# Performance work log

Measured on AMD Instinct MI355X. Metric: run time of the kernel, lower is better.

The kernel has to match this reference:

```python
import jax, jax.numpy as jnp
import numpy as np

N, E = 20000, 320000
IN, HID, R, HEADS = 128, 256, 4, 4
C = HID // HEADS  # per-head dim


def setup_inputs() -> dict:
    key = jax.random.key(0)
    ks = jax.random.split(key, 20)
    g = lambda k, s, sc=0.05: jax.random.normal(k, s, jnp.float32) * sc
    return {
        'x': g(ks[0], (N, IN), 1.0),
        'edge_index': jax.random.randint(ks[1], (2, E), 0, N),
        'edge_type': jax.random.randint(ks[2], (E,), 0, R),
        'h_prev': g(ks[3], (N, HID), 1.0),
        # RGCN layer 1: relation weights, root weight, bias
        'W1': g(ks[4], (R, IN, HID)), 'root1': g(ks[5], (IN, HID)), 'b1': jnp.zeros((HID,), jnp.float32),
        # RGCN layer 2
        'W2': g(ks[6], (R, HID, HID)), 'root2': g(ks[7], (HID, HID)), 'b2': jnp.zeros((HID,), jnp.float32),
        # TransformerConv linears (query/key/value/skip), each Linear(HID, HEADS*C)
        'Wq': g(ks[8], (HID, HID)), 'bq': jnp.zeros((HID,), jnp.float32),
        'Wk': g(ks[9], (HID, HID)), 'bk': jnp.zeros((HID,), jnp.float32),
        'Wv': g(ks[10], (HID, HID)), 'bv': jnp.zeros((HID,), jnp.float32),
        'Wskip': g(ks[11], (HID, HID)), 'bskip': jnp.zeros((HID,), jnp.float32),
        # GRUCell (torch layout: [3*HID, in], gates ordered r, z, n)
        'W_ih': g(ks[12], (3 * HID, HID)), 'b_ih': jnp.zeros((3 * HID,), jnp.float32),
        'W_hh': g(ks[13], (3 * HID, HID)), 'b_hh': jnp.zeros((3 * HID,), jnp.float32),
    }


def rgcn(x, src, dst, etype, W, Wroot, b):
    # PyG RGCNConv: out_i = x_i @ Wroot + b + sum_r mean_{j in N_r(i)} x_j @ W_r
    n = x.shape[0]
    out = x @ Wroot + b
    xs = x[src]  # [E, F_in]
    for r in range(W.shape[0]):  # small fixed relation count
        mask = (etype == r).astype(x.dtype)  # [E]
        msg = (xs @ W[r]) * mask[:, None]  # [E, F_out]
        agg = jax.ops.segment_sum(msg, dst, num_segments=n)
        cnt = jax.ops.segment_sum(mask, dst, num_segments=n)
        out = out + agg / jnp.maximum(cnt, 1.0)[:, None]
    return out


def transformer_conv(x, src, dst, Wq, bq, Wk, bk, Wv, bv, Wskip, bskip):
    # PyG TransformerConv, concat=True, root_weight=True
    n = x.shape[0]
    q = (x @ Wq + bq).reshape(n, HEADS, C)
    k = (x @ Wk + bk).reshape(n, HEADS, C)
    v = (x @ Wv + bv).reshape(n, HEADS, C)
    score = jnp.einsum('ehc,ehc->eh', q[dst], k[src]) * (1.0 / np.sqrt(C))  # [E, H]
    smax = jax.ops.segment_max(score, dst, num_segments=n)  # [N, H]
    ex = jnp.exp(score - smax[dst])
    denom = jax.ops.segment_sum(ex, dst, num_segments=n)
    alpha = ex / jnp.maximum(denom[dst], 1e-16)  # edge softmax per dst node
    out = jax.ops.segment_sum(alpha[:, :, None] * v[src], dst, num_segments=n)  # [N, H, C]
    return out.reshape(n, HEADS * C) + x @ Wskip + bskip


def gru_cell(xi, h, W_ih, b_ih, W_hh, b_hh):
    gi = xi @ W_ih.T + b_ih
    gh = h @ W_hh.T + b_hh
    ir, iz, inn = jnp.split(gi, 3, axis=1)
    hr, hz, hn = jnp.split(gh, 3, axis=1)
    r = jax.nn.sigmoid(ir + hr)
    z = jax.nn.sigmoid(iz + hz)
    nw = jnp.tanh(inn + r * hn)
    return (1.0 - z) * nw + z * h


def reference(x, edge_index, edge_type, h_prev, W1, root1, b1, W2, root2, b2,
              Wq, bq, Wk, bk, Wv, bv, Wskip, bskip, W_ih, b_ih, W_hh, b_hh):
    src, dst = edge_index[0], edge_index[1]
    h = jax.nn.relu(rgcn(x, src, dst, edge_type, W1, root1, b1))
    h = jax.nn.relu(rgcn(h, src, dst, edge_type, W2, root2, b2))
    h = transformer_conv(h, src, dst, Wq, bq, Wk, bk, Wv, bv, Wskip, bskip)
    h = gru_cell(h, h_prev, W_ih, b_ih, W_hh, b_hh)
    return h
```

## Files before the change

### kernel.cpp

```cpp
#include <hip/hip_runtime.h>
#include <hip/hip_bf16.h>
#include <stdint.h>

#define N_NODES 20000
#define E_EDGES 320000
#define IN_F    128
#define HIDF    256
#define R_REL   4
#define NRKEYS  (N_NODES*R_REL)
#define SCAN_BLOCKS 80

typedef __attribute__((ext_vector_type(8))) short  short8;
typedef __attribute__((ext_vector_type(4))) float  floatx4;

__device__ __forceinline__ float bf2f(__hip_bfloat16 v){ return __bfloat162float(v); }
__device__ __forceinline__ __hip_bfloat16 f2bf(float v){ return __float2bfloat16(v); }
__device__ __forceinline__ float bfbits2f(unsigned short u){ return __uint_as_float(((unsigned)u)<<16); }
__device__ __forceinline__ unsigned short f2bfbits(float v){
    __hip_bfloat16 h = __float2bfloat16(v);
    return *(unsigned short*)&h;
}
__device__ __forceinline__ unsigned pack_bf2(float a, float b){
    return (unsigned)f2bfbits(a) | ((unsigned)f2bfbits(b) << 16);
}

__device__ __forceinline__ void gload_lds16(const void* g, void* l)
{
    __builtin_amdgcn_global_load_lds((const __attribute__((address_space(1))) void*)g,
                                     (__attribute__((address_space(3))) void*)l, 16, 0, 0);
}

template<int N>
__device__ __forceinline__ void wait_vm()
{
    if constexpr (N == 0)      asm volatile("s_waitcnt vmcnt(0)" ::: "memory");
    else if constexpr (N == 3) asm volatile("s_waitcnt vmcnt(3)" ::: "memory");
    else if constexpr (N == 4) asm volatile("s_waitcnt vmcnt(4)" ::: "memory");
    else if constexpr (N == 5) asm volatile("s_waitcnt vmcnt(5)" ::: "memory");
    else                       asm volatile("s_waitcnt vmcnt(0)" ::: "memory");
}

__device__ __forceinline__ int2 xcd_swizzle()
{
    int gx = gridDim.x, gy = gridDim.y;
    int nwg = gx * gy;
    int lin = blockIdx.x + gx * blockIdx.y;
    int q = nwg >> 3, r = nwg & 7;
    int k = lin & 7, i = lin >> 3;
    int j = (k < r ? k*(q+1) : r*(q+1) + (k-r)*q) + i;
    return make_int2(j / gy, j % gy);
}

__global__ void count_kernel(const int* __restrict__ ei, const int* __restrict__ et,
                             int* __restrict__ cnt)
{
    int e = blockIdx.x*256 + threadIdx.x;
    if (e >= E_EDGES) return;
    int dst = ei[E_EDGES + e];
    atomicAdd(&cnt[dst*R_REL + et[e]], 1);
}

__global__ __launch_bounds__(1024) void scan_reduce_kernel(const int* __restrict__ cnt,
                                                           int* __restrict__ blocksum)
{
    int ix = blockIdx.x*1024 + threadIdx.x;
    int v = (ix < NRKEYS) ? cnt[ix] : 0;
    #pragma unroll
    for (int o=32;o>0;o>>=1) v += __shfl_xor(v, o, 64);
    __shared__ int wsum[16];
    int wave = threadIdx.x >> 6, lane = threadIdx.x & 63;
    if (lane == 0) wsum[wave] = v;
    __syncthreads();
    if (threadIdx.x == 0) {
        int s = 0;
        #pragma unroll
        for (int w=0;w<16;w++) s += wsum[w];
        blocksum[blockIdx.x] = s;
    }
}

__global__ __launch_bounds__(128) void scan_sums_kernel(const int* __restrict__ blocksum,
                                                        int* __restrict__ blockoff)
{
    __shared__ int s[128];
    int t = threadIdx.x;
    int v = (t < SCAN_BLOCKS) ? blocksum[t] : 0;
    s[t] = v; __syncthreads();
    for (int off=1; off<128; off<<=1) {
        int u = (t>=off) ? s[t-off] : 0;
        __syncthreads();
        s[t] += u;
        __syncthreads();
    }
    if (t < SCAN_BLOCKS) blockoff[t] = s[t] - v;
}

__global__ __launch_bounds__(1024) void scan_apply_kernel(const int* __restrict__ cnt,
                                                          const int* __restrict__ blockoff,
                                                          int* __restrict__ row_ptr,
                                                          int* __restrict__ cursor)
{
    __shared__ int s[1024];
    int t = threadIdx.x;
    int ix = blockIdx.x*1024 + t;
    int v = (ix < NRKEYS) ? cnt[ix] : 0;
    s[t] = v; __syncthreads();
    for (int off=1; off<1024; off<<=1) {
        int u = (t>=off) ? s[t-off] : 0;
        __syncthreads();
        s[t] += u;
        __syncthreads();
    }
    if (ix < NRKEYS) {
        int excl = blockoff[blockIdx.x] + s[t] - v;
        row_ptr[ix] = excl;
        cursor[ix]  = excl;
        if (ix == NRKEYS-1) row_ptr[NRKEYS] = excl + v;
    }
}

__global__ void fill_kernel(const int* __restrict__ ei, const int* __restrict__ et,
                            int* __restrict__ cursor, int* __restrict__ csr_src)
{
    int e = blockIdx.x*256 + threadIdx.x;
    if (e >= E_EDGES) return;
    int src = ei[e];
    int dst = ei[E_EDGES + e];
    int key = dst*R_REL + et[e];
    int pos = atomicAdd(&cursor[key], 1);
    csr_src[pos] = src;
}

__global__ void make_b1t(const float* __restrict__ root1,
                         const float* __restrict__ W1,
                         __hip_bfloat16* __restrict__ B1t)
{
    int idx = blockIdx.x*256 + threadIdx.x;
    if (idx >= 256*640) return;
    int n = idx / 640, k = idx % 640;
    float v;
    if (k < 128) v = root1[k*256 + n];
    else         v = W1[(k-128)*256 + n];
    B1t[idx] = f2bf(v);
}

__global__ void make_b2t(const float* __restrict__ root2,
                         const float* __restrict__ W2,
                         __hip_bfloat16* __restrict__ B2t)
{
    int idx = blockIdx.x*256 + threadIdx.x;
    if (idx >= 256*1280) return;
    int n = idx / 1280, k = idx % 1280;
    float v;
    if (k < 256) v = root2[k*256 + n];
    else         v = W2[(k-256)*256 + n];
    B2t[idx] = f2bf(v);
}

__global__ void make_b3t(const float* __restrict__ Wq, const float* __restrict__ Wk,
                         const float* __restrict__ Wv, const float* __restrict__ Wsk,
                         const float* __restrict__ bq, const float* __restrict__ bk,
                         const float* __restrict__ bv, const float* __restrict__ bsk,
                         __hip_bfloat16* __restrict__ B3t, float* __restrict__ bias3)
{
    int idx = blockIdx.x*256 + threadIdx.x;
    if (idx >= 1024*256) return;
    int n = idx / 256, k = idx % 256;
    int g = n >> 8, nn = n & 255;
    const float* W = (g==0)?Wq:(g==1)?Wk:(g==2)?Wv:Wsk;
    B3t[idx] = f2bf(W[k*256 + nn]);
    if (k == 0) {
        const float* B = (g==0)?bq:(g==1)?bk:(g==2)?bv:bsk;
        bias3[n] = B[nn];
    }
}

__global__ void cvt_f32_bf16(const float* __restrict__ in, __hip_bfloat16* __restrict__ out, int n)
{
    int i = blockIdx.x*256 + threadIdx.x;
    if (i < n) out[i] = f2bf(in[i]);
}

__global__ __launch_bounds__(256) void agg1_kernel(const float* __restrict__ x,
                                                   const int* __restrict__ row_ptr,
                                                   const int* __restrict__ csr_src,
                                                   __hip_bfloat16* __restrict__ A1)
{
    int b = blockIdx.x*4 + (threadIdx.x >> 6);
    int lane = threadIdx.x & 63;
    int i = b >> 2, r = b & 3;
    int e0 = row_ptr[b], e1 = row_ptr[b+1];
    float sx0=0.f,sy0=0.f, sx1=0.f,sy1=0.f, sx2=0.f,sy2=0.f, sx3=0.f,sy3=0.f;
    int e = e0;
    for (; e+4 <= e1; e += 4) {
        int i0=csr_src[e], i1=csr_src[e+1], i2=csr_src[e+2], i3=csr_src[e+3];
        float2 v0 = *(const float2*)(x + (size_t)i0*IN_F + lane*2);
        float2 v1 = *(const float2*)(x + (size_t)i1*IN_F + lane*2);
        float2 v2 = *(const float2*)(x + (size_t)i2*IN_F + lane*2);
        float2 v3 = *(const float2*)(x + (size_t)i3*IN_F + lane*2);
        sx0+=v0.x; sy0+=v0.y; sx1+=v1.x; sy1+=v1.y;
        sx2+=v2.x; sy2+=v2.y; sx3+=v3.x; sy3+=v3.y;
    }
    for (; e < e1; e++) {
        int i0 = csr_src[e];
        float2 v = *(const float2*)(x + (size_t)i0*IN_F + lane*2);
        sx0+=v.x; sy0+=v.y;
    }
    float sx = (sx0+sx1)+(sx2+sx3);
    float sy = (sy0+sy1)+(sy2+sy3);
    float inv = (e1>e0) ? 1.f/(float)(e1-e0) : 0.f;
    *(unsigned*)(A1 + (size_t)i*640 + 128 + r*128 + lane*2) = pack_bf2(sx*inv, sy*inv);
    if (r == 0) {
        float2 v = *(const float2*)(x + (size_t)i*IN_F + lane*2);
        *(unsigned*)(A1 + (size_t)i*640 + lane*2) = pack_bf2(v.x, v.y);
    }
}

__global__ __launch_bounds__(256) void agg2_kernel(const int* __restrict__ row_ptr,
                                                   const int* __restrict__ csr_src,
                                                   __hip_bfloat16* __restrict__ A2)
{
    int b = blockIdx.x*4 + (threadIdx.x >> 6);
    int lane = threadIdx.x & 63;
    int i = b >> 2, r = b & 3;
    int e0 = row_ptr[b], e1 = row_ptr[b+1];
    float a0=0.f,a1=0.f,a2=0.f,a3=0.f;
    float b0=0.f,b1=0.f,b2=0.f,b3=0.f;
    float c0=0.f,c1=0.f,c2=0.f,c3=0.f;
    float d0=0.f,d1=0.f,d2=0.f,d3=0.f;
    int e = e0;
    for (; e+4 <= e1; e += 4) {
        int i0=csr_src[e], i1=csr_src[e+1], i2=csr_src[e+2], i3=csr_src[e+3];
        ushort4 u0 = *(const ushort4*)(A2 + (size_t)i0*1280 + lane*4);
        ushort4 u1 = *(const ushort4*)(A2 + (size_t)i1*1280 + lane*4);
        ushort4 u2 = *(const ushort4*)(A2 + (size_t)i2*1280 + lane*4);
        ushort4 u3 = *(const ushort4*)(A2 + (size_t)i3*1280 + lane*4);
        a0+=bfbits2f(u0.x); a1+=bfbits2f(u0.y); a2+=bfbits2f(u0.z); a3+=bfbits2f(u0.w);
        b0+=bfbits2f(u1.x); b1+=bfbits2f(u1.y); b2+=bfbits2f(u1.z); b3+=bfbits2f(u1.w);
        c0+=bfbits2f(u2.x); c1+=bfbits2f(u2.y); c2+=bfbits2f(u2.z); c3+=bfbits2f(u2.w);
        d0+=bfbits2f(u3.x); d1+=bfbits2f(u3.y); d2+=bfbits2f(u3.z); d3+=bfbits2f(u3.w);
    }
    for (; e < e1; e++) {
        int i0 = csr_src[e];
        ushort4 u = *(const ushort4*)(A2 + (size_t)i0*1280 + lane*4);
        a0+=bfbits2f(u.x); a1+=bfbits2f(u.y); a2+=bfbits2f(u.z); a3+=bfbits2f(u.w);
    }
    float s0=(a0+b0)+(c0+d0), s1=(a1+b1)+(c1+d1), s2=(a2+b2)+(c2+d2), s3=(a3+b3)+(c3+d3);
    float inv = (e1>e0) ? 1.f/(float)(e1-e0) : 0.f;
    uint2 w;
    w.x = pack_bf2(s0*inv, s1*inv);
    w.y = pack_bf2(s2*inv, s3*inv);
    *(uint2*)(A2 + (size_t)i*1280 + 256 + r*256 + lane*4) = w;
}

template<int MI>
__device__ __forceinline__ void gemm_bt_body(const __hip_bfloat16* __restrict__ A, int lda,
                                             const __hip_bfloat16* __restrict__ Bt,
                                             const float* __restrict__ bias,
                                             __hip_bfloat16* __restrict__ C, int ldc,
                                             int M, int K, int relu,
                                             int tile_m, int tile_n,
                                             __hip_bfloat16* lds_a, __hip_bfloat16* lds_b)
{
    constexpr int A_ELEMS = MI*1024;
    constexpr int B_ELEMS = 4096;
    constexpr int L = MI/2 + 2;
    const int tid  = threadIdx.x;
    const int wave = tid >> 6;
    const int lane = tid & 63;
    const int wm = wave >> 1, wn = wave & 1;
    const int fm = lane & 15;
    const int q  = lane >> 4;
    const int sw = (q ^ ((fm >> 1) & 3)) * 8;

    floatx4 acc[MI][4];
    #pragma unroll
    for (int i=0;i<MI;i++)
        #pragma unroll
        for (int j=0;j<4;j++) acc[i][j] = (floatx4){0.f,0.f,0.f,0.f};

    const int srow   = lane >> 2;
    const int schunk = lane & 3;
    size_t a_goff[MI/2];
    #pragma unroll
    for (int s = 0; s < MI/2; ++s) {
        int r = (s*4 + wave)*16 + srow;
        int c = schunk ^ ((r >> 1) & 3);
        a_goff[s] = (size_t)min(tile_m + r, M-1)*lda + c*8;
    }
    size_t b_goff[2];
    #pragma unroll
    for (int s = 0; s < 2; ++s) {
        int r = (s*4 + wave)*16 + srow;
        int c = schunk ^ ((r >> 1) & 3);
        b_goff[s] = (size_t)(tile_n + r)*K + c*8;
    }

    const int nt = K >> 5;

    auto issue = [&](int t, int bufi) {
        const int kn = t << 5;
        #pragma unroll
        for (int s = 0; s < MI/2; ++s)
            gload_lds16(A + a_goff[s] + kn, lds_a + bufi*A_ELEMS + (s*4 + wave)*512);
        #pragma unroll
        for (int s = 0; s < 2; ++s)
            gload_lds16(Bt + b_goff[s] + kn, lds_b + bufi*B_ELEMS + (s*4 + wave)*512);
    };

    issue(0, 0);
    if (nt > 1) { issue(1, 1); wait_vm<L>(); }
    else        { wait_vm<0>(); }
    __builtin_amdgcn_s_barrier();

    int cur = 0, nx2 = 2;
    for (int t = 0; t < nt; ++t) {
        if (t + 2 < nt) issue(t + 2, nx2);

        const __hip_bfloat16* la = lds_a + cur*A_ELEMS;
        const __hip_bfloat16* lb = lds_b + cur*B_ELEMS;
        short8 afr[MI], bfr[4];
        #pragma unroll
        for (int i=0;i<MI;i++)
            afr[i] = *(const short8*)(la + (wm*(MI*16) + i*16 + fm)*32 + sw);
        #pragma unroll
        for (int j=0;j<4;j++)
            bfr[j] = *(const short8*)(lb + (wn*64 + j*16 + fm)*32 + sw);

        __builtin_amdgcn_s_setprio(1);
        #pragma unroll
        for (int i=0;i<MI;i++)
            #pragma unroll
            for (int j=0;j<4;j++)
                acc[i][j] = __builtin_amdgcn_mfma_f32_16x16x32_bf16(afr[i], bfr[j], acc[i][j], 0,0,0);
        __builtin_amdgcn_s_setprio(0);

        if (t + 1 < nt) {
            if (t + 2 < nt) wait_vm<L>();
            else            wait_vm<0>();
            __builtin_amdgcn_s_barrier();
            cur = (cur == 2) ? 0 : cur + 1;
            nx2 = (nx2 == 2) ? 0 : nx2 + 1;
        }
    }

    const int crow_base = tile_m + wm*(MI*16);
    const int ccol_base = tile_n + wn*64;
    #pragma unroll
    for (int i=0;i<MI;i++) {
        #pragma unroll
        for (int j=0;j<4;j++) {
            int c  = ccol_base + j*16 + fm;
            float bb = bias[c];
            #pragma unroll
            for (int rg=0; rg<4; rg++) {
                int r = crow_base + i*16 + q*4 + rg;
                if (r < M) {
                    float v = acc[i][j][rg] + bb;
                    if (relu) v = fmaxf(v, 0.f);
                    C[(size_t)r*ldc + c] = f2bf(v);
                }
            }
        }
    }
}

template<int MI>
__global__ __launch_bounds__(256) void gemm_bt_t(const __hip_bfloat16* __restrict__ A, int lda,
                                                 const __hip_bfloat16* __restrict__ Bt,
                                                 const float* __restrict__ bias,
                                                 __hip_bfloat16* __restrict__ C, int ldc,
                                                 int M, int K, int relu)
{
    __shared__ __align__(16) __hip_bfloat16 lds_a[3*MI*1024];
    __shared__ __align__(16) __hip_bfloat16 lds_b[3*4096];
    int2 xy = xcd_swizzle();
    gemm_bt_body<MI>(A, lda, Bt, bias, C, ldc, M, K, relu,
                     xy.x*(MI*32), xy.y*128, lds_a, lds_b);
}

__global__ __launch_bounds__(256) void gemm_gru_fused(
    const __hip_bfloat16* __restrict__ A0,
    const __hip_bfloat16* __restrict__ A1,
    const __hip_bfloat16* __restrict__ Bt0,
    const __hip_bfloat16* __restrict__ Bt1,
    const float* __restrict__ b_ih, const float* __restrict__ b_hh,
    const float* __restrict__ hprev, float* __restrict__ out)
{
    constexpr int BUF_ELEMS = 10240;
    __shared__ __align__(16) __hip_bfloat16 lds[3*BUF_ELEMS];
    int2 xy = xcd_swizzle();
    const int tile_m = xy.x * 64;
    const int c0     = xy.y * 32;
    const int tid = threadIdx.x, wave = tid >> 6, lane = tid & 63;
    const int fm = lane & 15, q = lane >> 4;
    const int sw = (q ^ ((fm >> 1) & 3)) * 8;

    const int sub = lane >> 2, ch = lane & 3;
    const __hip_bfloat16* gsrc[5];
    int dstoff[5];
    #pragma unroll
    for (int s = 0; s < 5; ++s) {
        int seg = wave*5 + s;
        if (seg < 8) {
            int fr = seg*16 + sub;
            int mat = fr >> 6, rl = fr & 63;
            int c = ch ^ ((fr >> 1) & 3);
            int grow = min(tile_m + rl, N_NODES-1);
            gsrc[s] = (mat ? A1 : A0) + (size_t)grow*256 + c*8;
            dstoff[s] = seg*512;
        } else {
            int fs = seg - 8;
            int fr = fs*16 + sub;
            int grp = fr >> 5, ri = fr & 31;
            int mat = grp >= 3, gate = mat ? grp-3 : grp;
            int c = ch ^ ((fr >> 1) & 3);
            int grow = gate*256 + c0 + ri;
            gsrc[s] = (mat ? Bt1 : Bt0) + (size_t)grow*256 + c*8;
            dstoff[s] = 4096 + fs*512;
        }
    }

    floatx4 acc[2][3][2];
    #pragma unroll
    for (int m=0;m<2;m++)
        #pragma unroll
        for (int g=0;g<3;g++)
            #pragma unroll
            for (int f=0;f<2;f++) acc[m][g][f] = (floatx4){0.f,0.f,0.f,0.f};

    auto issue = [&](int t, int bufi) {
        const int kn = t << 5;
        #pragma unroll
        for (int s = 0; s < 5; ++s)
            gload_lds16(gsrc[s] + kn, lds + bufi*BUF_ELEMS + dstoff[s]);
    };

    issue(0, 0);
    issue(1, 1);
    wait_vm<5>();
    __builtin_amdgcn_s_barrier();

    int cur = 0, nx2 = 2;
    #pragma unroll 1
    for (int t = 0; t < 8; ++t) {
        if (t + 2 < 8) issue(t + 2, nx2);

        const __hip_bfloat16* lb = lds + cur*BUF_ELEMS;
        short8 af[2], bf_[2][3][2];
        #pragma unroll
        for (int m=0;m<2;m++)
            af[m] = *(const short8*)(lb + (m*64 + wave*16 + fm)*32 + sw);
        #pragma unroll
        for (int m=0;m<2;m++)
            #pragma unroll
            for (int g=0;g<3;g++)
                #pragma unroll
                for (int f=0;f<2;f++)
                    bf_[m][g][f] = *(const short8*)(lb + 4096 + (((m*3+g)*32) + f*16 + fm)*32 + sw);

        __builtin_amdgcn_s_setprio(1);
        #pragma unroll
        for (int m=0;m<2;m++)
            #pragma unroll
            for (int g=0;g<3;g++)
                #pragma unroll
                for (int f=0;f<2;f++)
                    acc[m][g][f] = __builtin_amdgcn_mfma_f32_16x16x32_bf16(af[m], bf_[m][g][f], acc[m][g][f], 0,0,0);
        __builtin_amdgcn_s_setprio(0);

        if (t + 1 < 8) {
            if (t + 2 < 8) wait_vm<5>();
            else           wait_vm<0>();
            __builtin_amdgcn_s_barrier();
            cur = (cur == 2) ? 0 : cur + 1;
            nx2 = (nx2 == 2) ? 0 : nx2 + 1;
        }
    }

    #pragma unroll
    for (int f=0; f<2; ++f) {
        int c = c0 + f*16 + fm;
        float bir = b_ih[c], biz = b_ih[256+c], bin = b_ih[512+c];
        float bhr = b_hh[c], bhz = b_hh[256+c], bhn = b_hh[512+c];
        #pragma unroll
        for (int rg=0; rg<4; ++rg) {
            int r = tile_m + wave*16 + q*4 + rg;
            if (r < N_NODES) {
                float gir = acc[0][0][f][rg] + bir;
                float giz = acc[0][1][f][rg] + biz;
                float gin = acc[0][2][f][rg] + bin;
                float ghr = acc[1][0][f][rg] + bhr;
                float ghz = acc[1][1][f][rg] + bhz;
                float ghn = acc[1][2][f][rg] + bhn;
                float rr = 1.f/(1.f + __expf(-(gir + ghr)));
                float zz = 1.f/(1.f + __expf(-(giz + ghz)));
                float nn = tanhf(gin + rr*ghn);
                float h  = hprev[(size_t)r*256 + c];
                out[(size_t)r*256 + c] = (1.f - zz)*nn + zz*h;
            }
        }
    }
}

__global__ __launch_bounds__(256) void score_kernel(const __hip_bfloat16* __restrict__ qkvs,
                                                    const int* __restrict__ row_ptr,
                                                    const int* __restrict__ csr_src,
                                                    float* __restrict__ score)
{
    int i = blockIdx.x*4 + (threadIdx.x >> 6);
    int lane = threadIdx.x & 63;
    int h = lane >> 4, d4 = lane & 15;
    int e0 = row_ptr[i*R_REL], e1 = row_ptr[i*R_REL + R_REL];
    ushort4 qv = *(const ushort4*)(qkvs + (size_t)i*1024 + lane*4);
    float qx=bfbits2f(qv.x), qy=bfbits2f(qv.y), qz=bfbits2f(qv.z), qw=bfbits2f(qv.w);
    float* sp = score + (size_t)h*E_EDGES;
    int j = e0;
    for (; j+2 <= e1; j += 2) {
        int s0 = csr_src[j], s1 = csr_src[j+1];
        ushort4 k0 = *(const ushort4*)(qkvs + (size_t)s0*1024 + 256 + lane*4);
        ushort4 k1 = *(const ushort4*)(qkvs + (size_t)s1*1024 + 256 + lane*4);
        float d0 = qx*bfbits2f(k0.x)+qy*bfbits2f(k0.y)+qz*bfbits2f(k0.z)+qw*bfbits2f(k0.w);
        float d1 = qx*bfbits2f(k1.x)+qy*bfbits2f(k1.y)+qz*bfbits2f(k1.z)+qw*bfbits2f(k1.w);
        #pragma unroll
        for (int o=1;o<16;o<<=1){ d0 += __shfl_xor(d0,o,64); d1 += __shfl_xor(d1,o,64); }
        if (d4 == 0) { sp[j] = d0*0.125f; sp[j+1] = d1*0.125f; }
    }
    for (; j < e1; j++) {
        int s0 = csr_src[j];
        ushort4 k0 = *(const ushort4*)(qkvs + (size_t)s0*1024 + 256 + lane*4);
        float d0 = qx*bfbits2f(k0.x)+qy*bfbits2f(k0.y)+qz*bfbits2f(k0.z)+qw*bfbits2f(k0.w);
        #pragma unroll
        for (int o=1;o<16;o<<=1) d0 += __shfl_xor(d0,o,64);
        if (d4 == 0) sp[j] = d0*0.125f;
    }
}

__global__ __launch_bounds__(256) void attn_agg_kernel(const __hip_bfloat16* __restrict__ qkvs,
                                                       const float* __restrict__ score,
                                                       const int* __restrict__ row_ptr,
                                                       const int* __restrict__ csr_src,
                                                       __hip_bfloat16* __restrict__ hatt)
{
    int i = blockIdx.x*4 + (threadIdx.x >> 6);
    int lane = threadIdx.x & 63;
    int h  = lane >> 4;
    int d4 = lane & 15;
    int e0 = row_ptr[i*R_REL], e1 = row_ptr[i*R_REL + R_REL];
    int deg = e1 - e0;
    const float* sp = score + (size_t)h*E_EDGES + e0;

    float m = -1e30f;
    for (int j = d4; j < deg; j += 16) m = fmaxf(m, sp[j]);
    #pragma unroll
    for (int o=1;o<16;o<<=1) m = fmaxf(m, __shfl_xor(m, o, 64));

    float ssum = 0.f;
    for (int j = d4; j < deg; j += 16) ssum += __expf(sp[j] - m);
    #pragma unroll
    for (int o=1;o<16;o<<=1) ssum += __shfl_xor(ssum, o, 64);
    float inv = 1.f / fmaxf(ssum, 1e-16f);

    float ax=0.f, ay=0.f, az=0.f, aw=0.f;
    int j = 0;
    for (; j+4 <= deg; j += 4) {
        int s0=csr_src[e0+j], s1=csr_src[e0+j+1], s2=csr_src[e0+j+2], s3=csr_src[e0+j+3];
        float w0 = __expf(sp[j]   - m) * inv;
        float w1 = __expf(sp[j+1] - m) * inv;
        float w2 = __expf(sp[j+2] - m) * inv;
        float w3 = __expf(sp[j+3] - m) * inv;
        ushort4 u0 = *(const ushort4*)(qkvs + (size_t)s0*1024 + 512 + lane*4);
        ushort4 u1 = *(const ushort4*)(qkvs + (size_t)s1*1024 + 512 + lane*4);
        ushort4 u2 = *(const ushort4*)(qkvs + (size_t)s2*1024 + 512 + lane*4);
        ushort4 u3 = *(const ushort4*)(qkvs + (size_t)s3*1024 + 512 + lane*4);
        ax += w0*bfbits2f(u0.x) + w1*bfbits2f(u1.x) + w2*bfbits2f(u2.x) + w3*bfbits2f(u3.x);
        ay += w0*bfbits2f(u0.y) + w1*bfbits2f(u1.y) + w2*bfbits2f(u2.y) + w3*bfbits2f(u3.y);
        az += w0*bfbits2f(u0.z) + w1*bfbits2f(u1.z) + w2*bfbits2f(u2.z) + w3*bfbits2f(u3.z);
        aw += w0*bfbits2f(u0.w) + w1*bfbits2f(u1.w) + w2*bfbits2f(u2.w) + w3*bfbits2f(u3.w);
    }
    for (; j < deg; j++) {
        int s = csr_src[e0+j];
        float w = __expf(sp[j] - m) * inv;
        ushort4 u = *(const ushort4*)(qkvs + (size_t)s*1024 + 512 + lane*4);
        ax += w*bfbits2f(u.x); ay += w*bfbits2f(u.y);
        az += w*bfbits2f(u.z); aw += w*bfbits2f(u.w);
    }
    ushort4 sk = *(const ushort4*)(qkvs + (size_t)i*1024 + 768 + lane*4);
    uint2 w;
    w.x = pack_bf2(ax + bfbits2f(sk.x), ay + bfbits2f(sk.y));
    w.y = pack_bf2(az + bfbits2f(sk.z), aw + bfbits2f(sk.w));
    *(uint2*)(hatt + (size_t)i*256 + lane*4) = w;
}

extern "C" void kernel_launch(void* const* d_in, const int* in_sizes, int n_in,
                              void* d_out, int out_size, void* d_ws, size_t ws_size,
                              hipStream_t stream)
{
    const float* x       = (const float*)d_in[0];
    const int* edge_index= (const int*)d_in[1];
    const int* edge_type = (const int*)d_in[2];
    const float* hprev   = (const float*)d_in[3];
    const float* W1      = (const float*)d_in[4];
    const float* root1   = (const float*)d_in[5];
    const float* b1      = (const float*)d_in[6];
    const float* W2      = (const float*)d_in[7];
    const float* root2   = (const float*)d_in[8];
    const float* b2      = (const float*)d_in[9];
    const float* Wq      = (const float*)d_in[10];
    const float* bq      = (const float*)d_in[11];
    const float* Wk      = (const float*)d_in[12];
    const float* bk      = (const float*)d_in[13];
    const float* Wv      = (const float*)d_in[14];
    const float* bv      = (const float*)d_in[15];
    const float* Wskip   = (const float*)d_in[16];
    const float* bskip   = (const float*)d_in[17];
    const float* W_ih    = (const float*)d_in[18];
    const float* b_ih    = (const float*)d_in[19];
    const float* W_hh    = (const float*)d_in[20];
    const float* b_hh    = (const float*)d_in[21];

    char* ws = (char*)d_ws;
    size_t off = 0;
    auto take = [&](size_t bytes)->char* {
        char* p = ws + off;
        off = (off + bytes + 255) & ~(size_t)255;
        return p;
    };
    int* cnt        = (int*)take((size_t)NRKEYS*4);
    int* row_ptr    = (int*)take((size_t)(NRKEYS+1)*4);
    int* cursor     = (int*)take((size_t)NRKEYS*4);
    int* csr_src    = (int*)take((size_t)E_EDGES*4);
    int* blocksum   = (int*)take((size_t)SCAN_BLOCKS*4);
    int* blockoff   = (int*)take((size_t)(SCAN_BLOCKS+1)*4);
    float* score    = (float*)take((size_t)R_REL*E_EDGES*4);
    __hip_bfloat16* B1t   = (__hip_bfloat16*)take((size_t)256*640*2);
    __hip_bfloat16* B2t   = (__hip_bfloat16*)take((size_t)256*1280*2);
    __hip_bfloat16* B3t   = (__hip_bfloat16*)take((size_t)1024*256*2);
    __hip_bfloat16* Biht  = (__hip_bfloat16*)take((size_t)768*256*2);
    __hip_bfloat16* Bhht  = (__hip_bfloat16*)take((size_t)768*256*2);
    float*          bias3 = (float*)take((size_t)1024*4);
    __hip_bfloat16* hprev_bf = (__hip_bfloat16*)take((size_t)N_NODES*256*2);
    char* P1 = take((size_t)N_NODES*640*2);
    char* P2 = take((size_t)N_NODES*1536*2);

    __hip_bfloat16* A1   = (__hip_bfloat16*)P1;
    __hip_bfloat16* h2   = (__hip_bfloat16*)P1;
    __hip_bfloat16* hatt = (__hip_bfloat16*)P1;
    __hip_bfloat16* A2   = (__hip_bfloat16*)P2;
    __hip_bfloat16* qkvs = (__hip_bfloat16*)P2;

    hipMemsetAsync(cnt, 0, (size_t)NRKEYS*4, stream);
    count_kernel<<<(E_EDGES+255)/256, 256, 0, stream>>>(edge_index, edge_type, cnt);
    scan_reduce_kernel<<<SCAN_BLOCKS, 1024, 0, stream>>>(cnt, blocksum);
    scan_sums_kernel<<<1, 128, 0, stream>>>(blocksum, blockoff);
    scan_apply_kernel<<<SCAN_BLOCKS, 1024, 0, stream>>>(cnt, blockoff, row_ptr, cursor);
    fill_kernel<<<(E_EDGES+255)/256, 256, 0, stream>>>(edge_index, edge_type, cursor, csr_src);

    make_b1t<<<(256*640+255)/256, 256, 0, stream>>>(root1, W1, B1t);
    make_b2t<<<(256*1280+255)/256, 256, 0, stream>>>(root2, W2, B2t);
    make_b3t<<<(1024*256+255)/256, 256, 0, stream>>>(Wq, Wk, Wv, Wskip, bq, bk, bv, bskip, B3t, bias3);
    cvt_f32_bf16<<<(768*256+255)/256, 256, 0, stream>>>(W_ih, Biht, 768*256);
    cvt_f32_bf16<<<(768*256+255)/256, 256, 0, stream>>>(W_hh, Bhht, 768*256);
    cvt_f32_bf16<<<(N_NODES*256+255)/256, 256, 0, stream>>>(hprev, hprev_bf, N_NODES*256);

    agg1_kernel<<<NRKEYS/4, 256, 0, stream>>>(x, row_ptr, csr_src, A1);

    dim3 g12(313, 2);
    gemm_bt_t<2><<<g12, 256, 0, stream>>>(A1, 640, B1t, b1, A2, 1280, N_NODES, 640, 1);

    agg2_kernel<<<NRKEYS/4, 256, 0, stream>>>(row_ptr, csr_src, A2);

    gemm_bt_t<2><<<g12, 256, 0, stream>>>(A2, 1280, B2t, b2, h2, 256, N_NODES, 1280, 1);

    dim3 g3(157, 8);
    gemm_bt_t<4><<<g3, 256, 0, stream>>>(h2, 256, B3t, bias3, qkvs, 1024, N_NODES, 256, 0);

    score_kernel<<<N_NODES/4, 256, 0, stream>>>(qkvs, row_ptr, csr_src, score);
    attn_agg_kernel<<<N_NODES/4, 256, 0, stream>>>(qkvs, score, row_ptr, csr_src, hatt);

    gemm_gru_fused<<<dim3(313, 8), 256, 0, stream>>>(hatt, hprev_bf, Biht, Bhht,
                                                     b_ih, b_hh, hprev, (float*)d_out);
}
```

Measured before the change: 431.2 us.

## Widen fused GRU GEMM tile to 64 columns with 2x2 wave layout and double buffering

The fused GRU gate GEMM now computes 64 output columns per block instead of 32. The four waves are arranged 2x2, so each A fragment is reused across more MFMAs and the grid is halved. The LDS pipeline goes from triple to double buffering with an extra barrier before each refill, which may expose more load latency. tanhf is also replaced with an exp-based formula.

```diff
diff --git a/kernel.cpp b/kernel.cpp
--- a/kernel.cpp
+++ b/kernel.cpp
@@ -37,6 +37,7 @@
     else if constexpr (N == 3) asm volatile("s_waitcnt vmcnt(3)" ::: "memory");
     else if constexpr (N == 4) asm volatile("s_waitcnt vmcnt(4)" ::: "memory");
     else if constexpr (N == 5) asm volatile("s_waitcnt vmcnt(5)" ::: "memory");
+    else if constexpr (N == 8) asm volatile("s_waitcnt vmcnt(8)" ::: "memory");
     else                       asm volatile("s_waitcnt vmcnt(0)" ::: "memory");
 }
 
@@ -387,21 +388,22 @@
     const float* __restrict__ b_ih, const float* __restrict__ b_hh,
     const float* __restrict__ hprev, float* __restrict__ out)
 {
-    constexpr int BUF_ELEMS = 10240;
-    __shared__ __align__(16) __hip_bfloat16 lds[3*BUF_ELEMS];
+    constexpr int BUF_ELEMS = 16384;
+    __shared__ __align__(16) __hip_bfloat16 lds[2*BUF_ELEMS];
     int2 xy = xcd_swizzle();
     const int tile_m = xy.x * 64;
-    const int c0     = xy.y * 32;
+    const int c0     = xy.y * 64;
     const int tid = threadIdx.x, wave = tid >> 6, lane = tid & 63;
+    const int wm = wave >> 1, wn = wave & 1;
     const int fm = lane & 15, q = lane >> 4;
     const int sw = (q ^ ((fm >> 1) & 3)) * 8;
 
     const int sub = lane >> 2, ch = lane & 3;
-    const __hip_bfloat16* gsrc[5];
-    int dstoff[5];
-    #pragma unroll
-    for (int s = 0; s < 5; ++s) {
-        int seg = wave*5 + s;
+    const __hip_bfloat16* gsrc[8];
+    int dstoff[8];
+    #pragma unroll
+    for (int s = 0; s < 8; ++s) {
+        int seg = wave*8 + s;
         if (seg < 8) {
             int fr = seg*16 + sub;
             int mat = fr >> 6, rl = fr & 63;
@@ -412,7 +414,7 @@
         } else {
             int fs = seg - 8;
             int fr = fs*16 + sub;
-            int grp = fr >> 5, ri = fr & 31;
+            int grp = fr >> 6, ri = fr & 63;
             int mat = grp >= 3, gate = mat ? grp-3 : grp;
             int c = ch ^ ((fr >> 1) & 3);
             int grow = gate*256 + c0 + ri;
@@ -421,43 +423,44 @@
         }
     }
 
-    floatx4 acc[2][3][2];
+    floatx4 acc[2][3][2][2];
     #pragma unroll
     for (int m=0;m<2;m++)
         #pragma unroll
         for (int g=0;g<3;g++)
             #pragma unroll
-            for (int f=0;f<2;f++) acc[m][g][f] = (floatx4){0.f,0.f,0.f,0.f};
+            for (int i=0;i<2;i++)
+                #pragma unroll
+                for (int f=0;f<2;f++) acc[m][g][i][f] = (floatx4){0.f,0.f,0.f,0.f};
 
     auto issue = [&](int t, int bufi) {
         const int kn = t << 5;
         #pragma unroll
-        for (int s = 0; s < 5; ++s)
+        for (int s = 0; s < 8; ++s)
             gload_lds16(gsrc[s] + kn, lds + bufi*BUF_ELEMS + dstoff[s]);
     };
 
     issue(0, 0);
     issue(1, 1);
-    wait_vm<5>();
+    wait_vm<8>();
     __builtin_amdgcn_s_barrier();
 
-    int cur = 0, nx2 = 2;
     #pragma unroll 1
     for (int t = 0; t < 8; ++t) {
-        if (t + 2 < 8) issue(t + 2, nx2);
-
-        const __hip_bfloat16* lb = lds + cur*BUF_ELEMS;
-        short8 af[2], bf_[2][3][2];
+        const __hip_bfloat16* lb = lds + (t & 1)*BUF_ELEMS;
+        short8 af[2][2], bfr[2][3][2];
         #pragma unroll
         for (int m=0;m<2;m++)
-            af[m] = *(const short8*)(lb + (m*64 + wave*16 + fm)*32 + sw);
+            #pragma unroll
+            for (int i=0;i<2;i++)
+                af[m][i] = *(const short8*)(lb + (m*64 + wm*32 + i*16 + fm)*32 + sw);
         #pragma unroll
         for (int m=0;m<2;m++)
             #pragma unroll
             for (int g=0;g<3;g++)
                 #pragma unroll
                 for (int f=0;f<2;f++)
-                    bf_[m][g][f] = *(const short8*)(lb + 4096 + (((m*3+g)*32) + f*16 + fm)*32 + sw);
+                    bfr[m][g][f] = *(const short8*)(lb + 4096 + (((m*3+g)*64 + wn*32 + f*16 + fm)*32) + sw);
 
         __builtin_amdgcn_s_setprio(1);
         #pragma unroll
@@ -465,39 +468,45 @@
             #pragma unroll
             for (int g=0;g<3;g++)
                 #pragma unroll
-                for (int f=0;f<2;f++)
-                    acc[m][g][f] = __builtin_amdgcn_mfma_f32_16x16x32_bf16(af[m], bf_[m][g][f], acc[m][g][f], 0,0,0);
+                for (int i=0;i<2;i++)
+                    #pragma unroll
+                    for (int f=0;f<2;f++)
+                        acc[m][g][i][f] = __builtin_amdgcn_mfma_f32_16x16x32_bf16(af[m][i], bfr[m][g][f], acc[m][g][i][f], 0,0,0);
         __builtin_amdgcn_s_setprio(0);
 
         if (t + 1 < 8) {
-            if (t + 2 < 8) wait_vm<5>();
+            __builtin_amdgcn_s_barrier();
+            if (t + 2 < 8) { issue(t + 2, t & 1); wait_vm<8>(); }
             else           wait_vm<0>();
             __builtin_amdgcn_s_barrier();
-            cur = (cur == 2) ? 0 : cur + 1;
-            nx2 = (nx2 == 2) ? 0 : nx2 + 1;
         }
     }
 
     #pragma unroll
     for (int f=0; f<2; ++f) {
-        int c = c0 + f*16 + fm;
+        int c = c0 + wn*32 + f*16 + fm;
         float bir = b_ih[c], biz = b_ih[256+c], bin = b_ih[512+c];
         float bhr = b_hh[c], bhz = b_hh[256+c], bhn = b_hh[512+c];
         #pragma unroll
-        for (int rg=0; rg<4; ++rg) {
-            int r = tile_m + wave*16 + q*4 + rg;
-            if (r < N_NODES) {
-                float gir = acc[0][0][f][rg] + bir;
-                float giz = acc[0][1][f][rg] + biz;
-                float gin = acc[0][2][f][rg] + bin;
-                float ghr = acc[1][0][f][rg] + bhr;
-                float ghz = acc[1][1][f][rg] + bhz;
-                float ghn = acc[1][2][f][rg] + bhn;
-                float rr = 1.f/(1.f + __expf(-(gir + ghr)));
-                float zz = 1.f/(1.f + __expf(-(giz + ghz)));
-                float nn = tanhf(gin + rr*ghn);
-                float h  = hprev[(size_t)r*256 + c];
-                out[(size_t)r*256 + c] = (1.f - zz)*nn + zz*h;
+        for (int i=0; i<2; ++i) {
+            #pragma unroll
+            for (int rg=0; rg<4; ++rg) {
+                int r = tile_m + wm*32 + i*16 + q*4 + rg;
+                if (r < N_NODES) {
+                    float gir = acc[0][0][i][f][rg] + bir;
+                    float giz = acc[0][1][i][f][rg] + biz;
+                    float gin = acc[0][2][i][f][rg] + bin;
+                    float ghr = acc[1][0][i][f][rg] + bhr;
+                    float ghz = acc[1][1][i][f][rg] + bhz;
+                    float ghn = acc[1][2][i][f][rg] + bhn;
+                    float rr = 1.f/(1.f + __expf(-(gir + ghr)));
+                    float zz = 1.f/(1.f + __expf(-(giz + ghz)));
+                    float xn = gin + rr*ghn;
+                    float e2 = __expf(xn + xn);
+                    float nn = 1.f - 2.f/(e2 + 1.f);
+                    float h  = hprev[(size_t)r*256 + c];
+                    out[(size_t)r*256 + c] = (1.f - zz)*nn + zz*h;
+                }
             }
         }
     }
@@ -678,6 +687,6 @@
     score_kernel<<<N_NODES/4, 256, 0, stream>>>(qkvs, row_ptr, csr_src, score);
     attn_agg_kernel<<<N_NODES/4, 256, 0, stream>>>(qkvs, score, row_ptr, csr_src, hatt);
 
-    gemm_gru_fused<<<dim3(313, 8), 256, 0, stream>>>(hatt, hprev_bf, Biht, Bhht,
+    gemm_gru_fused<<<dim3(313, 4), 256, 0, stream>>>(hatt, hprev_bf, Biht, Bhht,
                                                      b_ih, b_hh, hprev, (float*)d_out);
 }
```

After: 426.4 us. No clear change (-1.1%).

## Restructure GRU GEMM to keep B resident in LDS and stream A from registers

Applied to the files above, without the earlier changes.

The fused GRU GEMM now uses 512-thread blocks covering 256 rows by 16 columns. It preloads the whole K-extent of the six weight slices into LDS once and loads A fragments straight from global memory into registers, replacing the triple-buffered LDS pipeline and its per-step barriers. The intent is to cut repeated loads of the weights and the synchronisation cost, at the price of more global A traffic and less latency hiding. Separately, x is converted to bf16 before the first aggregation to halve gather bandwidth, and tanh is replaced by an exp-based formula.

```diff
diff --git a/kernel.cpp b/kernel.cpp
--- a/kernel.cpp
+++ b/kernel.cpp
@@ -36,7 +36,6 @@
     if constexpr (N == 0)      asm volatile("s_waitcnt vmcnt(0)" ::: "memory");
     else if constexpr (N == 3) asm volatile("s_waitcnt vmcnt(3)" ::: "memory");
     else if constexpr (N == 4) asm volatile("s_waitcnt vmcnt(4)" ::: "memory");
-    else if constexpr (N == 5) asm volatile("s_waitcnt vmcnt(5)" ::: "memory");
     else                       asm volatile("s_waitcnt vmcnt(0)" ::: "memory");
 }
 
@@ -181,7 +180,7 @@
     if (i < n) out[i] = f2bf(in[i]);
 }
 
-__global__ __launch_bounds__(256) void agg1_kernel(const float* __restrict__ x,
+__global__ __launch_bounds__(256) void agg1_kernel(const __hip_bfloat16* __restrict__ xbf,
                                                    const int* __restrict__ row_ptr,
                                                    const int* __restrict__ csr_src,
                                                    __hip_bfloat16* __restrict__ A1)
@@ -194,26 +193,26 @@
     int e = e0;
     for (; e+4 <= e1; e += 4) {
         int i0=csr_src[e], i1=csr_src[e+1], i2=csr_src[e+2], i3=csr_src[e+3];
-        float2 v0 = *(const float2*)(x + (size_t)i0*IN_F + lane*2);
-        float2 v1 = *(const float2*)(x + (size_t)i1*IN_F + lane*2);
-        float2 v2 = *(const float2*)(x + (size_t)i2*IN_F + lane*2);
-        float2 v3 = *(const float2*)(x + (size_t)i3*IN_F + lane*2);
-        sx0+=v0.x; sy0+=v0.y; sx1+=v1.x; sy1+=v1.y;
-        sx2+=v2.x; sy2+=v2.y; sx3+=v3.x; sy3+=v3.y;
+        unsigned u0 = *(const unsigned*)(xbf + (size_t)i0*IN_F + lane*2);
+        unsigned u1 = *(const unsigned*)(xbf + (size_t)i1*IN_F + lane*2);
+        unsigned u2 = *(const unsigned*)(xbf + (size_t)i2*IN_F + lane*2);
+        unsigned u3 = *(const unsigned*)(xbf + (size_t)i3*IN_F + lane*2);
+        sx0+=bfbits2f((unsigned short)u0); sy0+=bfbits2f((unsigned short)(u0>>16));
+        sx1+=bfbits2f((unsigned short)u1); sy1+=bfbits2f((unsigned short)(u1>>16));
+        sx2+=bfbits2f((unsigned short)u2); sy2+=bfbits2f((unsigned short)(u2>>16));
+        sx3+=bfbits2f((unsigned short)u3); sy3+=bfbits2f((unsigned short)(u3>>16));
     }
     for (; e < e1; e++) {
         int i0 = csr_src[e];
-        float2 v = *(const float2*)(x + (size_t)i0*IN_F + lane*2);
-        sx0+=v.x; sy0+=v.y;
+        unsigned u = *(const unsigned*)(xbf + (size_t)i0*IN_F + lane*2);
+        sx0+=bfbits2f((unsigned short)u); sy0+=bfbits2f((unsigned short)(u>>16));
     }
     float sx = (sx0+sx1)+(sx2+sx3);
     float sy = (sy0+sy1)+(sy2+sy3);
     float inv = (e1>e0) ? 1.f/(float)(e1-e0) : 0.f;
     *(unsigned*)(A1 + (size_t)i*640 + 128 + r*128 + lane*2) = pack_bf2(sx*inv, sy*inv);
-    if (r == 0) {
-        float2 v = *(const float2*)(x + (size_t)i*IN_F + lane*2);
-        *(unsigned*)(A1 + (size_t)i*640 + lane*2) = pack_bf2(v.x, v.y);
-    }
+    if (r == 0)
+        *(unsigned*)(A1 + (size_t)i*640 + lane*2) = *(const unsigned*)(xbf + (size_t)i*IN_F + lane*2);
 }
 
 __global__ __launch_bounds__(256) void agg2_kernel(const int* __restrict__ row_ptr,
@@ -379,7 +378,7 @@
                      xy.x*(MI*32), xy.y*128, lds_a, lds_b);
 }
 
-__global__ __launch_bounds__(256) void gemm_gru_fused(
+__global__ __launch_bounds__(512, 4) void gemm_gru_fused(
     const __hip_bfloat16* __restrict__ A0,
     const __hip_bfloat16* __restrict__ A1,
     const __hip_bfloat16* __restrict__ Bt0,
@@ -387,39 +386,35 @@
     const float* __restrict__ b_ih, const float* __restrict__ b_hh,
     const float* __restrict__ hprev, float* __restrict__ out)
 {
-    constexpr int BUF_ELEMS = 10240;
-    __shared__ __align__(16) __hip_bfloat16 lds[3*BUF_ELEMS];
+    __shared__ __align__(16) __hip_bfloat16 ldsb[8*96*32];
     int2 xy = xcd_swizzle();
-    const int tile_m = xy.x * 64;
-    const int c0     = xy.y * 32;
+    const int tile_m = xy.x * 256;
+    const int c0     = xy.y * 16;
     const int tid = threadIdx.x, wave = tid >> 6, lane = tid & 63;
     const int fm = lane & 15, q = lane >> 4;
     const int sw = (q ^ ((fm >> 1) & 3)) * 8;
 
-    const int sub = lane >> 2, ch = lane & 3;
-    const __hip_bfloat16* gsrc[5];
-    int dstoff[5];
-    #pragma unroll
-    for (int s = 0; s < 5; ++s) {
-        int seg = wave*5 + s;
-        if (seg < 8) {
-            int fr = seg*16 + sub;
-            int mat = fr >> 6, rl = fr & 63;
-            int c = ch ^ ((fr >> 1) & 3);
-            int grow = min(tile_m + rl, N_NODES-1);
-            gsrc[s] = (mat ? A1 : A0) + (size_t)grow*256 + c*8;
-            dstoff[s] = seg*512;
-        } else {
-            int fs = seg - 8;
-            int fr = fs*16 + sub;
-            int grp = fr >> 5, ri = fr & 31;
-            int mat = grp >= 3, gate = mat ? grp-3 : grp;
-            int c = ch ^ ((fr >> 1) & 3);
-            int grow = gate*256 + c0 + ri;
-            gsrc[s] = (mat ? Bt1 : Bt0) + (size_t)grow*256 + c*8;
-            dstoff[s] = 4096 + fs*512;
+    {
+        const int sub = lane >> 2, ch = lane & 3;
+        const int t = wave;
+        #pragma unroll
+        for (int rg = 0; rg < 6; ++rg) {
+            int mat = rg >= 3, gate = mat ? rg - 3 : rg;
+            int kk = t*32 + (ch ^ ((sub >> 1) & 3))*8;
+            const __hip_bfloat16* src = (mat ? Bt1 : Bt0)
+                                      + (size_t)(gate*256 + c0 + sub)*256 + kk;
+            gload_lds16(src, ldsb + t*3072 + rg*512);
         }
     }
+
+    const int rowA = tile_m + wave*32;
+    const __hip_bfloat16* ap[2][2];
+    #pragma unroll
+    for (int m = 0; m < 2; ++m)
+        #pragma unroll
+        for (int rf = 0; rf < 2; ++rf)
+            ap[m][rf] = (m ? A1 : A0)
+                      + (size_t)min(rowA + rf*16 + fm, N_NODES-1)*256 + q*8;
 
     floatx4 acc[2][3][2];
     #pragma unroll
@@ -427,75 +422,58 @@
         #pragma unroll
         for (int g=0;g<3;g++)
             #pragma unroll
-            for (int f=0;f<2;f++) acc[m][g][f] = (floatx4){0.f,0.f,0.f,0.f};
-
-    auto issue = [&](int t, int bufi) {
-        const int kn = t << 5;
-        #pragma unroll
-        for (int s = 0; s < 5; ++s)
-            gload_lds16(gsrc[s] + kn, lds + bufi*BUF_ELEMS + dstoff[s]);
-    };
-
-    issue(0, 0);
-    issue(1, 1);
-    wait_vm<5>();
+            for (int rf=0;rf<2;rf++) acc[m][g][rf] = (floatx4){0.f,0.f,0.f,0.f};
+
+    wait_vm<0>();
     __builtin_amdgcn_s_barrier();
 
-    int cur = 0, nx2 = 2;
-    #pragma unroll 1
+    #pragma unroll
     for (int t = 0; t < 8; ++t) {
-        if (t + 2 < 8) issue(t + 2, nx2);
-
-        const __hip_bfloat16* lb = lds + cur*BUF_ELEMS;
-        short8 af[2], bf_[2][3][2];
+        short8 av[2][2];
         #pragma unroll
         for (int m=0;m<2;m++)
-            af[m] = *(const short8*)(lb + (m*64 + wave*16 + fm)*32 + sw);
+            #pragma unroll
+            for (int rf=0;rf<2;rf++)
+                av[m][rf] = *(const short8*)(ap[m][rf] + t*32);
+
+        short8 bfr[2][3];
+        #pragma unroll
+        for (int m=0;m<2;m++)
+            #pragma unroll
+            for (int g=0;g<3;g++)
+                bfr[m][g] = *(const short8*)(ldsb + t*3072 + (m*3+g)*512 + fm*32 + sw);
+
+        __builtin_amdgcn_s_setprio(1);
         #pragma unroll
         for (int m=0;m<2;m++)
             #pragma unroll
             for (int g=0;g<3;g++)
                 #pragma unroll
-                for (int f=0;f<2;f++)
-                    bf_[m][g][f] = *(const short8*)(lb + 4096 + (((m*3+g)*32) + f*16 + fm)*32 + sw);
-
-        __builtin_amdgcn_s_setprio(1);
-        #pragma unroll
-        for (int m=0;m<2;m++)
-            #pragma unroll
-            for (int g=0;g<3;g++)
-                #pragma unroll
-                for (int f=0;f<2;f++)
-                    acc[m][g][f] = __builtin_amdgcn_mfma_f32_16x16x32_bf16(af[m], bf_[m][g][f], acc[m][g][f], 0,0,0);
+                for (int rf=0;rf<2;rf++)
+                    acc[m][g][rf] = __builtin_amdgcn_mfma_f32_16x16x32_bf16(av[m][rf], bfr[m][g], acc[m][g][rf], 0,0,0);
         __builtin_amdgcn_s_setprio(0);
-
-        if (t + 1 < 8) {
-            if (t + 2 < 8) wait_vm<5>();
-            else           wait_vm<0>();
-            __builtin_amdgcn_s_barrier();
-            cur = (cur == 2) ? 0 : cur + 1;
-            nx2 = (nx2 == 2) ? 0 : nx2 + 1;
-        }
-    }
-
-    #pragma unroll
-    for (int f=0; f<2; ++f) {
-        int c = c0 + f*16 + fm;
-        float bir = b_ih[c], biz = b_ih[256+c], bin = b_ih[512+c];
-        float bhr = b_hh[c], bhz = b_hh[256+c], bhn = b_hh[512+c];
+    }
+
+    const int c = c0 + fm;
+    const float bir = b_ih[c], biz = b_ih[256+c], bin = b_ih[512+c];
+    const float bhr = b_hh[c], bhz = b_hh[256+c], bhn = b_hh[512+c];
+    #pragma unroll
+    for (int rf=0; rf<2; ++rf) {
         #pragma unroll
         for (int rg=0; rg<4; ++rg) {
-            int r = tile_m + wave*16 + q*4 + rg;
+            int r = rowA + rf*16 + q*4 + rg;
             if (r < N_NODES) {
-                float gir = acc[0][0][f][rg] + bir;
-                float giz = acc[0][1][f][rg] + biz;
-                float gin = acc[0][2][f][rg] + bin;
-                float ghr = acc[1][0][f][rg] + bhr;
-                float ghz = acc[1][1][f][rg] + bhz;
-                float ghn = acc[1][2][f][rg] + bhn;
+                float gir = acc[0][0][rf][rg] + bir;
+                float giz = acc[0][1][rf][rg] + biz;
+                float gin = acc[0][2][rf][rg] + bin;
+                float ghr = acc[1][0][rf][rg] + bhr;
+                float ghz = acc[1][1][rf][rg] + bhz;
+                float ghn = acc[1][2][rf][rg] + bhn;
                 float rr = 1.f/(1.f + __expf(-(gir + ghr)));
                 float zz = 1.f/(1.f + __expf(-(giz + ghz)));
-                float nn = tanhf(gin + rr*ghn);
+                float xn = gin + rr*ghn;
+                float e2 = __expf(xn + xn);
+                float nn = 1.f - 2.f/(e2 + 1.f);
                 float h  = hprev[(size_t)r*256 + c];
                 out[(size_t)r*256 + c] = (1.f - zz)*nn + zz*h;
             }
@@ -640,6 +618,7 @@
     __hip_bfloat16* Bhht  = (__hip_bfloat16*)take((size_t)768*256*2);
     float*          bias3 = (float*)take((size_t)1024*4);
     __hip_bfloat16* hprev_bf = (__hip_bfloat16*)take((size_t)N_NODES*256*2);
+    __hip_bfloat16* xbf      = (__hip_bfloat16*)take((size_t)N_NODES*IN_F*2);
     char* P1 = take((size_t)N_NODES*640*2);
     char* P2 = take((size_t)N_NODES*1536*2);
 
@@ -662,8 +641,9 @@
     cvt_f32_bf16<<<(768*256+255)/256, 256, 0, stream>>>(W_ih, Biht, 768*256);
     cvt_f32_bf16<<<(768*256+255)/256, 256, 0, stream>>>(W_hh, Bhht, 768*256);
     cvt_f32_bf16<<<(N_NODES*256+255)/256, 256, 0, stream>>>(hprev, hprev_bf, N_NODES*256);
-
-    agg1_kernel<<<NRKEYS/4, 256, 0, stream>>>(x, row_ptr, csr_src, A1);
+    cvt_f32_bf16<<<(N_NODES*IN_F+255)/256, 256, 0, stream>>>(x, xbf, N_NODES*IN_F);
+
+    agg1_kernel<<<NRKEYS/4, 256, 0, stream>>>(xbf, row_ptr, csr_src, A1);
 
     dim3 g12(313, 2);
     gemm_bt_t<2><<<g12, 256, 0, stream>>>(A1, 640, B1t, b1, A2, 1280, N_NODES, 640, 1);
@@ -678,6 +658,6 @@
     score_kernel<<<N_NODES/4, 256, 0, stream>>>(qkvs, row_ptr, csr_src, score);
     attn_agg_kernel<<<N_NODES/4, 256, 0, stream>>>(qkvs, score, row_ptr, csr_src, hatt);
 
-    gemm_gru_fused<<<dim3(313, 8), 256, 0, stream>>>(hatt, hprev_bf, Biht, Bhht,
+    gemm_gru_fused<<<dim3(79, 16), 512, 0, stream>>>(hatt, hprev_bf, Biht, Bhht,
                                                      b_ih, b_hh, hprev, (float*)d_out);
 }
```

Result: no change. 431.0 us (-0.0%).
